# Performance work log

Hardware: AMD Instinct MI355X
Metric: run time of the kernel (lower is better)

Reference implementation:

```python
import jax, jax.numpy as jnp
import numpy as np

SOFTMAX_TEMP = 0.01
CART_PIXEL_WIDTH = 256
CART_RESOLUTION = 0.2592


def zn_desc(desc):
    # desc: B x C x N. Zero-mean, unit-std over channel dim (torch.std default ddof=1).
    mean = jnp.mean(desc, axis=1, keepdims=True)
    std = jnp.std(desc, axis=1, keepdims=True, ddof=1)
    return (desc - mean) / std


def compute_2D_from_3D(coords):
    cart_min_range = (CART_PIXEL_WIDTH / 2 - 0.5) * CART_RESOLUTION
    u = (cart_min_range + coords[:, 1]) / CART_RESOLUTION
    v = (cart_min_range - coords[:, 0]) / CART_RESOLUTION
    return jnp.stack([u, v], axis=2)


def setup_inputs() -> dict:
    key = jax.random.key(0)
    B, C, N, H, W = 2, 256, 1024, 256, 256
    ks = jax.random.split(key, 4)
    tgt_coords = jax.random.normal(ks[0], (B, 3, H * W), jnp.float32) * 10.0
    tgt_weights = jax.random.uniform(ks[1], (B, 1, H, W), dtype=jnp.float32)
    src_desc_norm = zn_desc(jax.random.normal(ks[2], (B, C, N), jnp.float32))
    tgt_desc = jax.random.normal(ks[3], (B, C, H, W), jnp.float32)
    return {
        'geometry_img': jnp.zeros((1,), jnp.int32),
        'tgt_coords': tgt_coords,
        'tgt_2D': jnp.zeros((1,), jnp.int32),
        'tgt_weights': tgt_weights,
        'tgt_weights_dense': jnp.zeros((1,), jnp.int32),
        'src_desc_norm': src_desc_norm,
        'tgt_desc': tgt_desc,
        'tgt_desc_dense': jnp.zeros((1,), jnp.int32),
        'cam_calib': jnp.zeros((1,), jnp.int32),
        'window_size': 16,
    }


def reference(geometry_img, tgt_coords, tgt_2D, tgt_weights, tgt_weights_dense,
              src_desc_norm, tgt_desc, tgt_desc_dense, cam_calib, window_size):
    B, C = tgt_desc.shape[0], tgt_desc.shape[1]
    M = tgt_desc.shape[2] * tgt_desc.shape[3]
    N = src_desc_norm.shape[2]

    tgt_desc_flat = tgt_desc.reshape(B, C, M)
    tgt_desc_norm = zn_desc(tgt_desc_flat)

    # B x N x M similarity (ZNCC): src^T @ tgt / C
    match_vals = jnp.einsum('bcn,bcm->bnm', src_desc_norm, tgt_desc_norm) / float(C)
    soft_match_vals = jax.nn.softmax(match_vals / SOFTMAX_TEMP, axis=2)
    max_softmax = jnp.max(soft_match_vals, axis=(1, 2))  # (B,)

    # three weighted sums sharing the same softmax matrix
    pseudo_coords = jnp.einsum('bcm,bnm->bcn', tgt_coords, soft_match_vals)
    pseudo_weights = jnp.einsum('bcm,bnm->bcn', tgt_weights.reshape(B, 1, M), soft_match_vals)
    pseudo_descs = jnp.einsum('bcm,bnm->bcn', tgt_desc_flat, soft_match_vals)          # B x C x N

    pseudo_2D = compute_2D_from_3D(pseudo_coords)  # B x N x 2
    pseudo_descs = zn_desc(pseudo_descs)
    valid_pts = jnp.ones((B, 1, N), jnp.int32)
    return pseudo_coords, pseudo_weights, pseudo_descs, pseudo_2D, valid_pts, max_softmax
```

## Files before the change

kernel.cpp:

```cpp
#include <hip/hip_runtime.h>
#include <hip/hip_bf16.h>

#define Bb   2
#define Cc   256
#define Nn   1024
#define Mm   65536
#define VROWS 272
#define MSTEP 32

#define SCL_OFF  0L
#define TMC_OFF  524288L
#define TCM_OFF  67633152L
#define SNC_OFF  138936320L
#define PART_OFF 139984896L
#define PS_OFF   PART_OFF
#define PS2_OFF  (PART_OFF + 2097152L)

#define O_COORD 0L
#define O_W     6144L
#define O_DESC  8192L
#define O_P2D   532480L
#define O_VALID 536576L
#define O_MAXSM 538624L

using f32x4 = __attribute__((ext_vector_type(4))) float;
using s16x8 = __attribute__((ext_vector_type(8))) short;

__device__ inline unsigned short f2bf(float x) {
    union { float f; unsigned int u; } v; v.f = x;
    unsigned int r = v.u + 0x7FFFu + ((v.u >> 16) & 1u);
    return (unsigned short)(r >> 16);
}
__device__ inline float bf2f(unsigned short u) {
    union { unsigned int u; float f; } v; v.u = ((unsigned int)u) << 16;
    return v.f;
}
__device__ inline float exp2v(float x) {
    float r; asm("v_exp_f32 %0, %1" : "=v"(r) : "v"(x)); return r;
}
__device__ inline unsigned int cvtpk(float lo, float hi) {
    unsigned int r;
    asm("v_cvt_pk_bf16_f32 %0, %1, %2" : "=v"(r) : "v"(lo), "v"(hi));
    return r;
}

__device__ inline void gld_lds16(const unsigned short* g, unsigned short* l) {
    __builtin_amdgcn_global_load_lds(
        (const __attribute__((address_space(1))) unsigned int*)g,
        (__attribute__((address_space(3))) unsigned int*)l, 16, 0, 0);
}

__global__ void k_prep_tgt(const float* __restrict__ tgt,
                           unsigned short* __restrict__ tmc,
                           unsigned short* __restrict__ tcm,
                           float* __restrict__ ps,
                           float* __restrict__ ps2) {
    __shared__ float lds[64][65];
    __shared__ float sm[4][64], sm2[4][64];
    int b = blockIdx.z, cy = blockIdx.y, c0 = cy * 64;
    long m0 = (long)blockIdx.x * 64;
    int ty = threadIdx.x >> 6, tx = threadIdx.x & 63;
    float s = 0.f, s2 = 0.f;
    #pragma unroll
    for (int k = 0; k < 16; ++k) {
        int ci = 4 * k + ty;
        float v = tgt[((long)b * Cc + c0 + ci) * Mm + m0 + tx];
        lds[ci][tx] = v;
        s += v; s2 += v * v;
        tcm[((long)b * VROWS + c0 + ci) * Mm + m0 + tx] = f2bf(v);
    }
    sm[ty][tx] = s; sm2[ty][tx] = s2;
    __syncthreads();
    #pragma unroll
    for (int k = 0; k < 16; ++k) {
        int mi = 4 * k + ty;
        tmc[((long)b * Mm + m0 + mi) * Cc + c0 + tx] = f2bf(lds[tx][mi]);
    }
    if (ty == 0) {
        long o = ((long)b * 4 + cy) * Mm + m0 + tx;
        ps[o]  = (sm[0][tx] + sm[1][tx]) + (sm[2][tx] + sm[3][tx]);
        ps2[o] = (sm2[0][tx] + sm2[1][tx]) + (sm2[2][tx] + sm2[3][tx]);
    }
}

__global__ void k_stats(const float* __restrict__ ps,
                        const float* __restrict__ ps2,
                        const float* __restrict__ coords,
                        const float* __restrict__ weights,
                        float* __restrict__ scl,
                        unsigned short* __restrict__ tcm) {
    int b = blockIdx.y;
    long m = (long)blockIdx.x * 256 + threadIdx.x;
    float s = 0.f, s2 = 0.f;
    #pragma unroll
    for (int k = 0; k < 4; ++k) {
        long o = ((long)b * 4 + k) * Mm + m;
        s += ps[o]; s2 += ps2[o];
    }
    float var = fmaxf((s2 - s * s * (1.0f / Cc)) * (1.0f / (Cc - 1)), 1e-20f);
    scl[(long)b * Mm + m] = 1.4426950408889634f * rsqrtf(var) * (1.0f / (Cc * 0.01f));
    unsigned short* vrow = tcm + ((long)b * VROWS + 256) * Mm + m;
    #pragma unroll
    for (int i = 0; i < 3; ++i) vrow[(long)i * Mm] = f2bf(coords[((long)b * 3 + i) * Mm + m]);
    vrow[3L * Mm] = f2bf(weights[(long)b * Mm + m]);
    vrow[4L * Mm] = 0x3F80;
    #pragma unroll
    for (int i = 5; i < 16; ++i) vrow[(long)i * Mm] = 0;
}

__global__ void k_prep_src(const float* __restrict__ src, unsigned short* __restrict__ snc) {
    __shared__ float lds[64][65];
    int b = blockIdx.z, c0 = blockIdx.y * 64, n0 = blockIdx.x * 64;
    int ty = threadIdx.x >> 6, tx = threadIdx.x & 63;
    #pragma unroll
    for (int k = 0; k < 16; ++k)
        lds[4 * k + ty][tx] = src[((long)b * Cc + c0 + 4 * k + ty) * Nn + n0 + tx];
    __syncthreads();
    #pragma unroll
    for (int k = 0; k < 16; ++k) {
        int ni = 4 * k + ty;
        snc[((long)b * Nn + n0 + ni) * Cc + c0 + tx] = f2bf(lds[tx][ni]);
    }
}

__global__ __launch_bounds__(256, 1) void k_main(const unsigned short* __restrict__ tmc,
                                                 const unsigned short* __restrict__ tcm,
                                                 const unsigned short* __restrict__ snc,
                                                 const float* __restrict__ scl,
                                                 unsigned short* __restrict__ part,
                                                 float* __restrict__ zp,
                                                 float* __restrict__ pp,
                                                 int mcn) {
    __shared__ __align__(16) unsigned short kb[2][8192];
    __shared__ __align__(16) unsigned short vb[2][8704];
    __shared__ __align__(16) unsigned short pbuf[4][4][16][40];

    int w = threadIdx.x >> 6, lane = threadIdx.x & 63;
    int l15 = lane & 15, lg = lane >> 4;
    int b = blockIdx.z, nt = blockIdx.y, mc = blockIdx.x;
    int nb = nt * 256 + w * 64;
    int mchunk = Mm / mcn;
    int nit = mchunk / MSTEP;
    long mbase = (long)mc * mchunk;

    s16x8 qf[4][8];
    #pragma unroll
    for (int st = 0; st < 4; ++st) {
        const unsigned short* qp = snc + ((long)b * Nn + nb + st * 16 + l15) * Cc + lg * 8;
        #pragma unroll
        for (int cc = 0; cc < 8; ++cc) qf[st][cc] = *(const s16x8*)(qp + cc * 32);
    }

    f32x4 acc[4][17];
    #pragma unroll
    for (int st = 0; st < 4; ++st)
        #pragma unroll
        for (int t = 0; t < 17; ++t) acc[st][t] = (f32x4){0.f, 0.f, 0.f, 0.f};
    float pmax[4] = {0.f, 0.f, 0.f, 0.f};

    const unsigned short* tmcb = tmc + (long)b * Mm * Cc;
    const unsigned short* tcmb = tcm + (long)b * VROWS * (long)Mm;
    const unsigned short* ksrc[4];
    #pragma unroll
    for (int i = 0; i < 4; ++i) {
        int ins = w * 4 + i;
        int row = 2 * ins + (lane >> 5);
        int gs  = (lane & 31) ^ (row & 7);
        ksrc[i] = tmcb + (mbase + row) * Cc + gs * 8;
    }
    const unsigned short* vsrc[5];
    int vj = ((lane & 3) ^ ((lane >> 3) & 3)) * 8;
    #pragma unroll
    for (int i = 0; i < 5; ++i) {
        int ins = (i < 4) ? (w * 4 + i) : 16;
        int row = ins * 16 + (lane >> 2);
        vsrc[i] = tcmb + (long)row * Mm + mbase + vj;
    }

    const float* sclb = scl + (long)b * Mm;

    auto stage = [&](int d) {
        unsigned short* kd = kb[d];
        unsigned short* vd = vb[d];
        #pragma unroll
        for (int i = 0; i < 4; ++i) gld_lds16(ksrc[i], kd + (w * 4 + i) * 512);
        #pragma unroll
        for (int i = 0; i < 4; ++i) gld_lds16(vsrc[i], vd + (w * 4 + i) * 512);
        if (w == 3) gld_lds16(vsrc[4], vd + 16 * 512);
        #pragma unroll
        for (int i = 0; i < 4; ++i) ksrc[i] += MSTEP * Cc;
        #pragma unroll
        for (int i = 0; i < 5; ++i) vsrc[i] += MSTEP;
    };

    int ksw = (l15 & 7) << 3;
    int vsw = (lg ^ ((l15 >> 1) & 3)) * 8;

    stage(0);
    __syncthreads();

    for (int s = 0; s < nit; ++s) {
        int cur = s & 1;
        if (s + 1 < nit) stage(cur ^ 1);
        const unsigned short* kbc = kb[cur];
        const unsigned short* vbc = vb[cur];
        long m0 = mbase + (long)s * MSTEP;
        float4 sc0 = *(const float4*)(sclb + m0 + lg * 4);
        float4 sc1 = *(const float4*)(sclb + m0 + 16 + lg * 4);

        #pragma unroll
        for (int t = 0; t < 2; ++t) {
            f32x4 dA = (f32x4){0.f, 0.f, 0.f, 0.f};
            f32x4 dB = (f32x4){0.f, 0.f, 0.f, 0.f};
            f32x4 dC = (f32x4){0.f, 0.f, 0.f, 0.f};
            f32x4 dD = (f32x4){0.f, 0.f, 0.f, 0.f};
            const unsigned short* kr = kbc + (t * 16 + l15) * Cc;
            #pragma unroll
            for (int cc = 0; cc < 8; ++cc) {
                s16x8 kf = *(const s16x8*)(kr + ((cc * 32 + lg * 8) ^ ksw));
                dA = __builtin_amdgcn_mfma_f32_16x16x32_bf16(kf, qf[0][cc], dA, 0, 0, 0);
                dB = __builtin_amdgcn_mfma_f32_16x16x32_bf16(kf, qf[1][cc], dB, 0, 0, 0);
                dC = __builtin_amdgcn_mfma_f32_16x16x32_bf16(kf, qf[2][cc], dC, 0, 0, 0);
                dD = __builtin_amdgcn_mfma_f32_16x16x32_bf16(kf, qf[3][cc], dD, 0, 0, 0);
            }
            float4 sc = t ? sc1 : sc0;
            #pragma unroll
            for (int st = 0; st < 4; ++st) {
                f32x4 d = (st == 0) ? dA : (st == 1) ? dB : (st == 2) ? dC : dD;
                float p0 = exp2v(d.x * sc.x);
                float p1 = exp2v(d.y * sc.y);
                float p2 = exp2v(d.z * sc.z);
                float p3 = exp2v(d.w * sc.w);
                pmax[st] = fmaxf(pmax[st], fmaxf(fmaxf(p0, p1), fmaxf(p2, p3)));
                unsigned long long pk =
                    (unsigned long long)cvtpk(p0, p1) | ((unsigned long long)cvtpk(p2, p3) << 32);
                *(unsigned long long*)&pbuf[w][st][l15][t * 16 + lg * 4] = pk;
            }
        }
        s16x8 pfA = *(const s16x8*)&pbuf[w][0][l15][lg * 8];
        s16x8 pfB = *(const s16x8*)&pbuf[w][1][l15][lg * 8];
        s16x8 pfC = *(const s16x8*)&pbuf[w][2][l15][lg * 8];
        s16x8 pfD = *(const s16x8*)&pbuf[w][3][l15][lg * 8];
        #pragma unroll
        for (int t = 0; t < 17; ++t) {
            s16x8 vf = *(const s16x8*)(vbc + (t * 16 + l15) * MSTEP + vsw);
            acc[0][t] = __builtin_amdgcn_mfma_f32_16x16x32_bf16(vf, pfA, acc[0][t], 0, 0, 0);
            acc[1][t] = __builtin_amdgcn_mfma_f32_16x16x32_bf16(vf, pfB, acc[1][t], 0, 0, 0);
            acc[2][t] = __builtin_amdgcn_mfma_f32_16x16x32_bf16(vf, pfC, acc[2][t], 0, 0, 0);
            acc[3][t] = __builtin_amdgcn_mfma_f32_16x16x32_bf16(vf, pfD, acc[3][t], 0, 0, 0);
        }
        __syncthreads();
    }

    #pragma unroll
    for (int st = 0; st < 4; ++st) {
        float pt = fmaxf(pmax[st], __shfl_xor(pmax[st], 16));
        pt = fmaxf(pt, __shfl_xor(pt, 32));
        long zi = ((long)(b * mcn + mc)) * Nn + nb + st * 16;
        if (lg == 1) zp[zi + l15] = acc[st][16].x;
        if (lane < 16) pp[zi + lane] = pt;
        unsigned short* po = part + (((long)(b * mcn + mc) * Nn) + nb + st * 16 + l15) * VROWS;
        #pragma unroll
        for (int t = 0; t < 17; ++t) {
            f32x4 a = acc[st][t];
            unsigned long long pk =
                (unsigned long long)cvtpk(a.x, a.y) | ((unsigned long long)cvtpk(a.z, a.w) << 32);
            *(unsigned long long*)&po[t * 16 + lg * 4] = pk;
        }
    }
}

__global__ void k_epi(const unsigned short* __restrict__ part,
                      const float* __restrict__ zp,
                      const float* __restrict__ pp,
                      float* __restrict__ out,
                      int mcn) {
    int w = threadIdx.x >> 6, lane = threadIdx.x & 63;
    int bn = blockIdx.x * 4 + w;
    int b = bn >> 10, n = bn & 1023;

    float Z = 0.f, pm = 0.f;
    for (int mc = 0; mc < mcn; ++mc) {
        long zi = ((long)(b * mcn + mc)) * Nn + n;
        Z += zp[zi];
        pm = fmaxf(pm, pp[zi]);
    }
    float invZ = 1.0f / Z;

    float dv[4], s1 = 0.f, s2 = 0.f;
    #pragma unroll
    for (int k = 0; k < 4; ++k) {
        int c = lane + 64 * k;
        float s = 0.f;
        for (int mc = 0; mc < mcn; ++mc)
            s += bf2f(part[((long)(b * mcn + mc) * Nn + n) * VROWS + c]);
        float d = s * invZ;
        dv[k] = d; s1 += d; s2 += d * d;
    }
    #pragma unroll
    for (int off = 1; off < 64; off <<= 1) { s1 += __shfl_xor(s1, off); s2 += __shfl_xor(s2, off); }
    float mean = s1 * (1.0f / 256.0f);
    float var = fmaxf((s2 - 256.0f * mean * mean) * (1.0f / 255.0f), 1e-20f);
    float istd = 1.0f / sqrtf(var);
    #pragma unroll
    for (int k = 0; k < 4; ++k)
        out[O_DESC + ((long)b * Cc + lane + 64 * k) * Nn + n] = (dv[k] - mean) * istd;

    float ex = 0.f;
    if (lane < 4) {
        int c = 256 + lane;
        for (int mc = 0; mc < mcn; ++mc)
            ex += bf2f(part[((long)(b * mcn + mc) * Nn + n) * VROWS + c]);
        ex *= invZ;
    }
    float pc0 = __shfl(ex, 0), pc1 = __shfl(ex, 1), pc2 = __shfl(ex, 2), wv = __shfl(ex, 3);
    if (lane == 0) {
        out[O_COORD + ((long)b * 3 + 0) * Nn + n] = pc0;
        out[O_COORD + ((long)b * 3 + 1) * Nn + n] = pc1;
        out[O_COORD + ((long)b * 3 + 2) * Nn + n] = pc2;
        out[O_W + (long)b * Nn + n] = wv;
        const float cmin = 33.048f;
        out[O_P2D + ((long)b * Nn + n) * 2 + 0] = (cmin + pc1) * (1.0f / 0.2592f);
        out[O_P2D + ((long)b * Nn + n) * 2 + 1] = (cmin - pc0) * (1.0f / 0.2592f);
        out[O_VALID + (long)b * Nn + n] = 1.0f;
        atomicMax((unsigned int*)out + O_MAXSM + b, __float_as_uint(pm * invZ));
    }
}

extern "C" void kernel_launch(void* const* d_in, const int* in_sizes, int n_in,
                              void* d_out, int out_size, void* d_ws, size_t ws_size,
                              hipStream_t stream) {
    const float* tgt_coords  = (const float*)d_in[1];
    const float* tgt_weights = (const float*)d_in[3];
    const float* src_desc    = (const float*)d_in[5];
    const float* tgt_desc    = (const float*)d_in[6];

    char* ws = (char*)d_ws;
    float* scl           = (float*)(ws + SCL_OFF);
    unsigned short* tmc  = (unsigned short*)(ws + TMC_OFF);
    unsigned short* tcm  = (unsigned short*)(ws + TCM_OFF);
    unsigned short* snc  = (unsigned short*)(ws + SNC_OFF);
    unsigned short* part = (unsigned short*)(ws + PART_OFF);
    float* ps            = (float*)(ws + PS_OFF);
    float* ps2           = (float*)(ws + PS2_OFF);
    float* out           = (float*)d_out;

    long need32 = PART_OFF + (long)Bb * 32 * Nn * VROWS * 2 + 2L * Bb * 32 * Nn * 4;
    int mcn = (ws_size >= (size_t)need32) ? 32 : 16;
    long zp_off = PART_OFF + (long)Bb * mcn * Nn * VROWS * 2;
    long pp_off = zp_off + (long)Bb * mcn * Nn * 4;
    float* zp = (float*)(ws + zp_off);
    float* pp = (float*)(ws + pp_off);

    k_prep_tgt<<<dim3(Mm / 64, Cc / 64, Bb), 256, 0, stream>>>(tgt_desc, tmc, tcm, ps, ps2);
    k_stats<<<dim3(Mm / 256, Bb), 256, 0, stream>>>(ps, ps2, tgt_coords, tgt_weights, scl, tcm);
    k_prep_src<<<dim3(Nn / 64, Cc / 64, Bb), 256, 0, stream>>>(src_desc, snc);
    k_main<<<dim3(mcn, Nn / 256, Bb), 256, 0, stream>>>(tmc, tcm, snc, scl, part, zp, pp, mcn);
    (void)hipMemsetAsync((char*)d_out + O_MAXSM * 4, 0, 2 * sizeof(float), stream);
    k_epi<<<dim3((Bb * Nn) / 4), 256, 0, stream>>>(part, zp, pp, out, mcn);
}
```

Measured before the change: 327.3 us.

## Software-pipeline PV matmul one step behind QK and softmax

Restructures the main loop so each iteration runs the P·V accumulation for the previous tile, then the QK scores and exp for the current tile. The V buffer becomes triple-buffered and the P buffer double-buffered, so the previous tile's data survives across the barrier. The aim is to let MFMA work overlap the exp/convert latency and give the scheduler independent instruction streams. In exchange it uses more LDS and adds register pressure on an already heavy accumulator set.

```diff
diff --git a/kernel.cpp b/kernel.cpp
--- a/kernel.cpp
+++ b/kernel.cpp
@@ -132,8 +132,8 @@
                                                  float* __restrict__ pp,
                                                  int mcn) {
     __shared__ __align__(16) unsigned short kb[2][8192];
-    __shared__ __align__(16) unsigned short vb[2][8704];
-    __shared__ __align__(16) unsigned short pbuf[4][4][16][40];
+    __shared__ __align__(16) unsigned short vb[3][8704];
+    __shared__ __align__(16) unsigned short pbuf[2][4][4][16][40];
 
     int w = threadIdx.x >> 6, lane = threadIdx.x & 63;
     int l15 = lane & 15, lg = lane >> 4;
@@ -179,9 +179,9 @@
 
     const float* sclb = scl + (long)b * Mm;
 
-    auto stage = [&](int d) {
-        unsigned short* kd = kb[d];
-        unsigned short* vd = vb[d];
+    auto stage = [&](int kd_i, int vd_i) {
+        unsigned short* kd = kb[kd_i];
+        unsigned short* vd = vb[vd_i];
         #pragma unroll
         for (int i = 0; i < 4; ++i) gld_lds16(ksrc[i], kd + (w * 4 + i) * 512);
         #pragma unroll
@@ -196,17 +196,34 @@
     int ksw = (l15 & 7) << 3;
     int vsw = (lg ^ ((l15 >> 1) & 3)) * 8;
 
-    stage(0);
+    auto pv_step = [&](int sp) {
+        const unsigned short* vbc = vb[sp % 3];
+        const unsigned short (*pr)[4][16][40] = pbuf[sp & 1];
+        s16x8 pfA = *(const s16x8*)&pr[w][0][l15][lg * 8];
+        s16x8 pfB = *(const s16x8*)&pr[w][1][l15][lg * 8];
+        s16x8 pfC = *(const s16x8*)&pr[w][2][l15][lg * 8];
+        s16x8 pfD = *(const s16x8*)&pr[w][3][l15][lg * 8];
+        #pragma unroll
+        for (int t = 0; t < 17; ++t) {
+            s16x8 vf = *(const s16x8*)(vbc + (t * 16 + l15) * MSTEP + vsw);
+            acc[0][t] = __builtin_amdgcn_mfma_f32_16x16x32_bf16(vf, pfA, acc[0][t], 0, 0, 0);
+            acc[1][t] = __builtin_amdgcn_mfma_f32_16x16x32_bf16(vf, pfB, acc[1][t], 0, 0, 0);
+            acc[2][t] = __builtin_amdgcn_mfma_f32_16x16x32_bf16(vf, pfC, acc[2][t], 0, 0, 0);
+            acc[3][t] = __builtin_amdgcn_mfma_f32_16x16x32_bf16(vf, pfD, acc[3][t], 0, 0, 0);
+        }
+    };
+
+    stage(0, 0);
     __syncthreads();
 
     for (int s = 0; s < nit; ++s) {
-        int cur = s & 1;
-        if (s + 1 < nit) stage(cur ^ 1);
-        const unsigned short* kbc = kb[cur];
-        const unsigned short* vbc = vb[cur];
+        if (s + 1 < nit) stage((s + 1) & 1, (s + 1) % 3);
+        const unsigned short* kbc = kb[s & 1];
         long m0 = mbase + (long)s * MSTEP;
         float4 sc0 = *(const float4*)(sclb + m0 + lg * 4);
         float4 sc1 = *(const float4*)(sclb + m0 + 16 + lg * 4);
+
+        if (s) pv_step(s - 1);
 
         #pragma unroll
         for (int t = 0; t < 2; ++t) {
@@ -234,23 +251,12 @@
                 pmax[st] = fmaxf(pmax[st], fmaxf(fmaxf(p0, p1), fmaxf(p2, p3)));
                 unsigned long long pk =
                     (unsigned long long)cvtpk(p0, p1) | ((unsigned long long)cvtpk(p2, p3) << 32);
-                *(unsigned long long*)&pbuf[w][st][l15][t * 16 + lg * 4] = pk;
+                *(unsigned long long*)&pbuf[s & 1][w][st][l15][t * 16 + lg * 4] = pk;
             }
         }
-        s16x8 pfA = *(const s16x8*)&pbuf[w][0][l15][lg * 8];
-        s16x8 pfB = *(const s16x8*)&pbuf[w][1][l15][lg * 8];
-        s16x8 pfC = *(const s16x8*)&pbuf[w][2][l15][lg * 8];
-        s16x8 pfD = *(const s16x8*)&pbuf[w][3][l15][lg * 8];
-        #pragma unroll
-        for (int t = 0; t < 17; ++t) {
-            s16x8 vf = *(const s16x8*)(vbc + (t * 16 + l15) * MSTEP + vsw);
-            acc[0][t] = __builtin_amdgcn_mfma_f32_16x16x32_bf16(vf, pfA, acc[0][t], 0, 0, 0);
-            acc[1][t] = __builtin_amdgcn_mfma_f32_16x16x32_bf16(vf, pfB, acc[1][t], 0, 0, 0);
-            acc[2][t] = __builtin_amdgcn_mfma_f32_16x16x32_bf16(vf, pfC, acc[2][t], 0, 0, 0);
-            acc[3][t] = __builtin_amdgcn_mfma_f32_16x16x32_bf16(vf, pfD, acc[3][t], 0, 0, 0);
-        }
         __syncthreads();
     }
+    pv_step(nit - 1);
 
     #pragma unroll
     for (int st = 0; st < 4; ++st) {
```

New measurement: 335.3 us. 2.5% more time.

## Halve per-wave query tile in main kernel to allow two blocks per CU

Applied to the files above, without the earlier changes.

Each wave now handles 32 source points instead of 64, which halves the query fragments, accumulators and P buffer per wave, and the grid doubles along N. Launch bounds go from 1 to 2 blocks per CU to raise occupancy and latency hiding. Global load addressing switches from 64-bit pointers to 32-bit offsets to save registers. In exchange, each K/V tile is loaded from global memory twice as often because fewer query rows share it, which raises memory traffic and lowers MFMA reuse per LDS fetch.

```diff
diff --git a/kernel.cpp b/kernel.cpp
--- a/kernel.cpp
+++ b/kernel.cpp
@@ -123,7 +123,7 @@
     }
 }
 
-__global__ __launch_bounds__(256, 1) void k_main(const unsigned short* __restrict__ tmc,
+__global__ __launch_bounds__(256, 2) void k_main(const unsigned short* __restrict__ tmc,
                                                  const unsigned short* __restrict__ tcm,
                                                  const unsigned short* __restrict__ snc,
                                                  const float* __restrict__ scl,
@@ -133,48 +133,48 @@
                                                  int mcn) {
     __shared__ __align__(16) unsigned short kb[2][8192];
     __shared__ __align__(16) unsigned short vb[2][8704];
-    __shared__ __align__(16) unsigned short pbuf[4][4][16][40];
+    __shared__ __align__(16) unsigned short pbuf[4][2][16][40];
 
     int w = threadIdx.x >> 6, lane = threadIdx.x & 63;
     int l15 = lane & 15, lg = lane >> 4;
     int b = blockIdx.z, nt = blockIdx.y, mc = blockIdx.x;
-    int nb = nt * 256 + w * 64;
+    int nb = nt * 128 + w * 32;
     int mchunk = Mm / mcn;
     int nit = mchunk / MSTEP;
     long mbase = (long)mc * mchunk;
 
-    s16x8 qf[4][8];
-    #pragma unroll
-    for (int st = 0; st < 4; ++st) {
+    s16x8 qf[2][8];
+    #pragma unroll
+    for (int st = 0; st < 2; ++st) {
         const unsigned short* qp = snc + ((long)b * Nn + nb + st * 16 + l15) * Cc + lg * 8;
         #pragma unroll
         for (int cc = 0; cc < 8; ++cc) qf[st][cc] = *(const s16x8*)(qp + cc * 32);
     }
 
-    f32x4 acc[4][17];
-    #pragma unroll
-    for (int st = 0; st < 4; ++st)
+    f32x4 acc[2][17];
+    #pragma unroll
+    for (int st = 0; st < 2; ++st)
         #pragma unroll
         for (int t = 0; t < 17; ++t) acc[st][t] = (f32x4){0.f, 0.f, 0.f, 0.f};
-    float pmax[4] = {0.f, 0.f, 0.f, 0.f};
+    float pmax[2] = {0.f, 0.f};
 
     const unsigned short* tmcb = tmc + (long)b * Mm * Cc;
     const unsigned short* tcmb = tcm + (long)b * VROWS * (long)Mm;
-    const unsigned short* ksrc[4];
+    unsigned koff[4];
     #pragma unroll
     for (int i = 0; i < 4; ++i) {
         int ins = w * 4 + i;
         int row = 2 * ins + (lane >> 5);
         int gs  = (lane & 31) ^ (row & 7);
-        ksrc[i] = tmcb + (mbase + row) * Cc + gs * 8;
-    }
-    const unsigned short* vsrc[5];
+        koff[i] = (unsigned)((mbase + row) * Cc + gs * 8);
+    }
+    unsigned voff[5];
     int vj = ((lane & 3) ^ ((lane >> 3) & 3)) * 8;
     #pragma unroll
     for (int i = 0; i < 5; ++i) {
         int ins = (i < 4) ? (w * 4 + i) : 16;
         int row = ins * 16 + (lane >> 2);
-        vsrc[i] = tcmb + (long)row * Mm + mbase + vj;
+        voff[i] = (unsigned)((long)row * Mm + mbase + vj);
     }
 
     const float* sclb = scl + (long)b * Mm;
@@ -183,14 +183,14 @@
         unsigned short* kd = kb[d];
         unsigned short* vd = vb[d];
         #pragma unroll
-        for (int i = 0; i < 4; ++i) gld_lds16(ksrc[i], kd + (w * 4 + i) * 512);
-        #pragma unroll
-        for (int i = 0; i < 4; ++i) gld_lds16(vsrc[i], vd + (w * 4 + i) * 512);
-        if (w == 3) gld_lds16(vsrc[4], vd + 16 * 512);
-        #pragma unroll
-        for (int i = 0; i < 4; ++i) ksrc[i] += MSTEP * Cc;
-        #pragma unroll
-        for (int i = 0; i < 5; ++i) vsrc[i] += MSTEP;
+        for (int i = 0; i < 4; ++i) gld_lds16(tmcb + koff[i], kd + (w * 4 + i) * 512);
+        #pragma unroll
+        for (int i = 0; i < 4; ++i) gld_lds16(tcmb + voff[i], vd + (w * 4 + i) * 512);
+        if (w == 3) gld_lds16(tcmb + voff[4], vd + 16 * 512);
+        #pragma unroll
+        for (int i = 0; i < 4; ++i) koff[i] += MSTEP * Cc;
+        #pragma unroll
+        for (int i = 0; i < 5; ++i) voff[i] += MSTEP;
     };
 
     int ksw = (l15 & 7) << 3;
@@ -212,21 +212,17 @@
         for (int t = 0; t < 2; ++t) {
             f32x4 dA = (f32x4){0.f, 0.f, 0.f, 0.f};
             f32x4 dB = (f32x4){0.f, 0.f, 0.f, 0.f};
-            f32x4 dC = (f32x4){0.f, 0.f, 0.f, 0.f};
-            f32x4 dD = (f32x4){0.f, 0.f, 0.f, 0.f};
             const unsigned short* kr = kbc + (t * 16 + l15) * Cc;
             #pragma unroll
             for (int cc = 0; cc < 8; ++cc) {
                 s16x8 kf = *(const s16x8*)(kr + ((cc * 32 + lg * 8) ^ ksw));
                 dA = __builtin_amdgcn_mfma_f32_16x16x32_bf16(kf, qf[0][cc], dA, 0, 0, 0);
                 dB = __builtin_amdgcn_mfma_f32_16x16x32_bf16(kf, qf[1][cc], dB, 0, 0, 0);
-                dC = __builtin_amdgcn_mfma_f32_16x16x32_bf16(kf, qf[2][cc], dC, 0, 0, 0);
-                dD = __builtin_amdgcn_mfma_f32_16x16x32_bf16(kf, qf[3][cc], dD, 0, 0, 0);
             }
             float4 sc = t ? sc1 : sc0;
             #pragma unroll
-            for (int st = 0; st < 4; ++st) {
-                f32x4 d = (st == 0) ? dA : (st == 1) ? dB : (st == 2) ? dC : dD;
+            for (int st = 0; st < 2; ++st) {
+                f32x4 d = st ? dB : dA;
                 float p0 = exp2v(d.x * sc.x);
                 float p1 = exp2v(d.y * sc.y);
                 float p2 = exp2v(d.z * sc.z);
@@ -239,21 +235,17 @@
         }
         s16x8 pfA = *(const s16x8*)&pbuf[w][0][l15][lg * 8];
         s16x8 pfB = *(const s16x8*)&pbuf[w][1][l15][lg * 8];
-        s16x8 pfC = *(const s16x8*)&pbuf[w][2][l15][lg * 8];
-        s16x8 pfD = *(const s16x8*)&pbuf[w][3][l15][lg * 8];
         #pragma unroll
         for (int t = 0; t < 17; ++t) {
             s16x8 vf = *(const s16x8*)(vbc + (t * 16 + l15) * MSTEP + vsw);
             acc[0][t] = __builtin_amdgcn_mfma_f32_16x16x32_bf16(vf, pfA, acc[0][t], 0, 0, 0);
             acc[1][t] = __builtin_amdgcn_mfma_f32_16x16x32_bf16(vf, pfB, acc[1][t], 0, 0, 0);
-            acc[2][t] = __builtin_amdgcn_mfma_f32_16x16x32_bf16(vf, pfC, acc[2][t], 0, 0, 0);
-            acc[3][t] = __builtin_amdgcn_mfma_f32_16x16x32_bf16(vf, pfD, acc[3][t], 0, 0, 0);
         }
         __syncthreads();
     }
 
     #pragma unroll
-    for (int st = 0; st < 4; ++st) {
+    for (int st = 0; st < 2; ++st) {
         float pt = fmaxf(pmax[st], __shfl_xor(pmax[st], 16));
         pt = fmaxf(pt, __shfl_xor(pt, 32));
         long zi = ((long)(b * mcn + mc)) * Nn + nb + st * 16;
@@ -355,7 +347,7 @@
     k_prep_tgt<<<dim3(Mm / 64, Cc / 64, Bb), 256, 0, stream>>>(tgt_desc, tmc, tcm, ps, ps2);
     k_stats<<<dim3(Mm / 256, Bb), 256, 0, stream>>>(ps, ps2, tgt_coords, tgt_weights, scl, tcm);
     k_prep_src<<<dim3(Nn / 64, Cc / 64, Bb), 256, 0, stream>>>(src_desc, snc);
-    k_main<<<dim3(mcn, Nn / 256, Bb), 256, 0, stream>>>(tmc, tcm, snc, scl, part, zp, pp, mcn);
+    k_main<<<dim3(mcn, Nn / 128, Bb), 256, 0, stream>>>(tmc, tcm, snc, scl, part, zp, pp, mcn);
     (void)hipMemsetAsync((char*)d_out + O_MAXSM * 4, 0, 2 * sizeof(float), stream);
     k_epi<<<dim3((Bb * Nn) / 4), 256, 0, stream>>>(part, zp, pp, out, mcn);
 }
```

Result: faster. 285.9 us (-12.7%).
